# Kernel tuning notes

Hardware: AMD Instinct MI355X
Metric: run time of the kernel (lower is better)

Reference implementation:

```python
import jax, jax.numpy as jnp
import numpy as np

D_MODEL, D_HIDDEN, N_EXPERTS, TOP_K = 1024, 2048, 8, 2


def setup_inputs() -> dict:
    key = jax.random.key(0)
    ks = jax.random.split(key, 8)
    s_in = 1.0 / np.sqrt(D_MODEL)
    s_hid = 1.0 / np.sqrt(D_HIDDEN)
    return {
        "x": jax.random.normal(ks[0], (1, 2048, D_MODEL), dtype=jnp.float32),
        # stacked expert weights, stored (in, out) so y = x @ W + b
        "W1": jax.random.normal(ks[1], (N_EXPERTS, D_MODEL, D_HIDDEN), dtype=jnp.float32) * s_in,
        "b1": jnp.zeros((N_EXPERTS, D_HIDDEN), dtype=jnp.float32),
        "W2": jax.random.normal(ks[2], (N_EXPERTS, D_MODEL, D_HIDDEN), dtype=jnp.float32) * s_in,
        "b2": jnp.zeros((N_EXPERTS, D_HIDDEN), dtype=jnp.float32),
        "Wo": jax.random.normal(ks[3], (N_EXPERTS, D_HIDDEN, D_MODEL), dtype=jnp.float32) * s_hid,
        "bo": jnp.zeros((N_EXPERTS, D_MODEL), dtype=jnp.float32),
        "Wr": jax.random.normal(ks[4], (D_MODEL, N_EXPERTS), dtype=jnp.float32) * s_in,
        "br": jnp.zeros((N_EXPERTS,), dtype=jnp.float32),
    }


def reference(x, W1, b1, W2, b2, Wo, bo, Wr, br):
    B, S, D = x.shape
    T = B * S
    xf = x.reshape(T, D)

    # router
    logits = xf @ Wr + br                      # [T, E]
    probs = jax.nn.softmax(logits, axis=-1)
    topk_probs, topk_idx = jax.lax.top_k(probs, TOP_K)  # [T, K]

    # combine weights: c[t, e] = sum_k topk_probs[t, k] * 1[topk_idx[t, k] == e]
    c = jnp.zeros((T, N_EXPERTS), dtype=xf.dtype)
    c = c.at[jnp.arange(T)[:, None], topk_idx].add(topk_probs)  # [T, E]

    # per-expert SwiGLU FFN applied densely, then masked-combined (same math
    # as the original gather/scatter loop since c[t,e]=0 for unrouted experts)
    h = jnp.einsum('td,edh->eth', xf, W1) + b1[:, None, :]   # [E, T, H]
    g = jnp.einsum('td,edh->eth', xf, W2) + b2[:, None, :]
    y = jnp.einsum('eth,ehd->etd', h * jax.nn.silu(g), Wo) + bo[:, None, :]
    out = jnp.einsum('etd,te->td', y, c).reshape(B, S, D)

    probs_mean = probs.mean(axis=0)
    lb_loss = (probs_mean * probs_mean).sum() * N_EXPERTS
    return out, lb_loss
```

## Files before the change

kernel.cpp:

```cpp
#include <hip/hip_runtime.h>
#include <hip/hip_bf16.h>

#define T_TOK 2048
#define DM 1024
#define DH 2048
#define NE 8
#define MT_MAX 40

using bf16x8 = __attribute__((ext_vector_type(8))) short;
using f32x4  = __attribute__((ext_vector_type(4))) float;

__device__ __forceinline__ unsigned short f2bf(float f) {
  union { float f; unsigned u; } v; v.f = f;
  unsigned r = v.u + 0x7FFFu + ((v.u >> 16) & 1u);
  return (unsigned short)(r >> 16);
}
__device__ __forceinline__ unsigned pk2(float a, float b) {
  return (unsigned)f2bf(a) | ((unsigned)f2bf(b) << 16);
}

#define GLOAD16(gsrc, ldst)                                                        \
  __builtin_amdgcn_global_load_lds(                                                \
      (const __attribute__((address_space(1))) unsigned int*)(gsrc),               \
      (__attribute__((address_space(3))) unsigned int*)(ldst), 16, 0, 0)

__global__ void k_init(int* __restrict__ cnt) {
  if (threadIdx.x < NE) cnt[threadIdx.x] = 0;
}

__global__ __launch_bounds__(256) void k_router(
    const float* __restrict__ x, const float* __restrict__ Wr, const float* __restrict__ br,
    int* __restrict__ cnt, int* __restrict__ idx, float* __restrict__ wgt,
    int* __restrict__ t2r, float* __restrict__ probs, unsigned short* __restrict__ xb)
{
  const int wave = threadIdx.x >> 6, l = threadIdx.x & 63;
  const int t = blockIdx.x * 4 + wave;
  float xv[16];
#pragma unroll
  for (int i = 0; i < 16; ++i) xv[i] = x[t*DM + l + 64*i];
#pragma unroll
  for (int i = 0; i < 16; ++i) xb[t*DM + l + 64*i] = f2bf(xv[i]);

  float acc[8] = {0.f,0.f,0.f,0.f,0.f,0.f,0.f,0.f};
#pragma unroll
  for (int i = 0; i < 16; ++i) {
    const float4* wp = (const float4*)&Wr[(size_t)(l + 64*i)*NE];
    float4 wa = wp[0], wb = wp[1];
    acc[0] += xv[i]*wa.x; acc[1] += xv[i]*wa.y; acc[2] += xv[i]*wa.z; acc[3] += xv[i]*wa.w;
    acc[4] += xv[i]*wb.x; acc[5] += xv[i]*wb.y; acc[6] += xv[i]*wb.z; acc[7] += xv[i]*wb.w;
  }
#pragma unroll
  for (int e = 0; e < 8; ++e) {
#pragma unroll
    for (int off = 32; off; off >>= 1) acc[e] += __shfl_xor(acc[e], off, 64);
    acc[e] += br[e];
  }
  float mx = acc[0];
#pragma unroll
  for (int e = 1; e < 8; ++e) mx = fmaxf(mx, acc[e]);
  float p[8], s = 0.f;
#pragma unroll
  for (int e = 0; e < 8; ++e) { p[e] = expf(acc[e] - mx); s += p[e]; }
  float inv = 1.f / s;
#pragma unroll
  for (int e = 0; e < 8; ++e) p[e] *= inv;

  int e0 = 0; float p0 = p[0];
#pragma unroll
  for (int e = 1; e < 8; ++e) if (p[e] > p0) { p0 = p[e]; e0 = e; }
  int e1 = -1; float p1 = -1.f;
#pragma unroll
  for (int e = 0; e < 8; ++e) { if (e == e0) continue; if (p[e] > p1) { p1 = p[e]; e1 = e; } }

  if (l == 0) {
#pragma unroll
    for (int e = 0; e < 8; ++e) probs[t*NE + e] = p[e];
    int pos0 = atomicAdd(&cnt[e0], 1);
    idx[e0*T_TOK + pos0] = t; wgt[e0*T_TOK + pos0] = p0;
    t2r[t*2 + 0] = e0*T_TOK + pos0;
    int pos1 = atomicAdd(&cnt[e1], 1);
    idx[e1*T_TOK + pos1] = t; wgt[e1*T_TOK + pos1] = p1;
    t2r[t*2 + 1] = e1*T_TOK + pos1;
  }
}

__global__ __launch_bounds__(256) void k_finalize(
    const int* __restrict__ cnt, int* __restrict__ rb,
    const float* __restrict__ probs, float* __restrict__ out,
    int* __restrict__ MTp, int* __restrict__ mtab)
{
  __shared__ float red[8][256];
  const int tid = threadIdx.x;
  float s[8] = {0.f,0.f,0.f,0.f,0.f,0.f,0.f,0.f};
  for (int t = tid; t < T_TOK; t += 256) {
#pragma unroll
    for (int e = 0; e < 8; ++e) s[e] += probs[t*NE + e];
  }
#pragma unroll
  for (int e = 0; e < 8; ++e) red[e][tid] = s[e];
  __syncthreads();
  for (int w = 128; w > 0; w >>= 1) {
    if (tid < w) {
#pragma unroll
      for (int e = 0; e < 8; ++e) red[e][tid] += red[e][tid + w];
    }
    __syncthreads();
  }
  if (tid == 0) {
    float lb = 0.f;
#pragma unroll
    for (int e = 0; e < 8; ++e) {
      float mean = red[e][0] * (1.f / T_TOK);
      lb += mean * mean;
    }
    out[2097152] = lb * NE;
    int r = 0, mc = 0;
#pragma unroll
    for (int e = 0; e < 8; ++e) {
      rb[e] = r; r += cnt[e];
      int nmt = (cnt[e] + 127) / 128;
      for (int j = 0; j < nmt; ++j) mtab[mc++] = (e << 16) | j;
    }
    *MTp = mc;
  }
}

__global__ __launch_bounds__(256) void k_convT(
    const float* __restrict__ in, unsigned short* __restrict__ outT,
    int R, int C, int nnt)
{
  const int e = blockIdx.z;
  const int r0 = blockIdx.y * 64, c0 = blockIdx.x * 64;
  __shared__ float t[64][65];
  const int tid = threadIdx.x;
  const int lr = tid >> 4, lc = (tid & 15) * 4;
#pragma unroll
  for (int i = 0; i < 4; ++i) {
    float4 v = *(const float4*)&in[((size_t)e*R + r0 + lr + i*16)*C + c0 + lc];
    t[lr + i*16][lc+0] = v.x; t[lr + i*16][lc+1] = v.y;
    t[lr + i*16][lc+2] = v.z; t[lr + i*16][lc+3] = v.w;
  }
  __syncthreads();
  const int oc = tid >> 3;
  const int od = (tid & 7) * 8;
  const size_t base2 = ((size_t)e*128 + (size_t)(r0 >> 6)*nnt + (c0 >> 8)) * 16384
                     + (size_t)(c0 & 255) * 64;
#pragma unroll
  for (int i = 0; i < 2; ++i) {
    int c = oc + i*32;
    uint4 v;
    v.x = pk2(t[od+0][c], t[od+1][c]);
    v.y = pk2(t[od+2][c], t[od+3][c]);
    v.z = pk2(t[od+4][c], t[od+5][c]);
    v.w = pk2(t[od+6][c], t[od+7][c]);
    *(uint4*)&outT[base2 + (size_t)c*64 + od] = v;
  }
}

#define TM1 128
#define TN1 64
#define BKK 64

__global__ __launch_bounds__(256) void k_ffn1b(
    const unsigned short* __restrict__ xb,
    const unsigned short* __restrict__ W1T, const float* __restrict__ b1,
    const unsigned short* __restrict__ W2T, const float* __restrict__ b2,
    const int* __restrict__ cnt, const int* __restrict__ rbp,
    const int* __restrict__ idx, unsigned short* __restrict__ act,
    const int* __restrict__ MTp, const int* __restrict__ mtab)
{
  const int mtg = blockIdx.y;
  if (mtg >= *MTp) return;
  const int code = mtab[mtg];
  const int e = code >> 16, mt = code & 0xffff;
  const int Me = cnt[e];
  const int m0 = mt * TM1;
  const int nt = blockIdx.x;
  const int n0 = nt * TN1;

  __shared__ __align__(16) unsigned short As[TM1*BKK];
  __shared__ __align__(16) unsigned short Bh[TN1*BKK];
  __shared__ __align__(16) unsigned short Bg[TN1*BKK];
  __shared__ int toks[TM1];

  const int tid = threadIdx.x;
  if (tid < TM1) toks[tid] = idx[e*T_TOK + min(m0 + tid, Me - 1)];
  __syncthreads();

  const int lane = tid & 63;
  const int wave = tid >> 6;
  const int wm = wave >> 1, wn = wave & 1;
  const int row16 = lane & 15, kg = lane >> 4;
  const int sl = lane & 7;
  const int lr = lane >> 3;

  const unsigned short* asrc[4];
#pragma unroll
  for (int i = 0; i < 4; ++i) {
    int r = (wave*4 + i)*8 + lr;
    asrc[i] = &xb[(size_t)toks[r]*DM + ((sl ^ (r & 7)) * 8)];
  }
  const unsigned short *bsrc1[2], *bsrc2[2];
  const int nt256 = n0 >> 8, nsub = n0 & 255;
#pragma unroll
  for (int j = 0; j < 2; ++j) {
    int r = (wave*2 + j)*8 + lr;
    size_t gb = ((size_t)e*128 + nt256)*16384 + (size_t)(nsub + r)*64 + ((sl ^ (r & 7)) * 8);
    bsrc1[j] = &W1T[gb]; bsrc2[j] = &W2T[gb];
  }

  f32x4 ah[4][2], ag[4][2];
#pragma unroll
  for (int i = 0; i < 4; ++i)
#pragma unroll
    for (int j = 0; j < 2; ++j) { ah[i][j] = 0.f; ag[i][j] = 0.f; }

  for (int k0 = 0; k0 < DM; k0 += BKK) {
    const size_t bko = (size_t)k0 * 2048;
#pragma unroll
    for (int i = 0; i < 4; ++i)
      GLOAD16(asrc[i] + k0, &As[(wave*4 + i)*512]);
#pragma unroll
    for (int j = 0; j < 2; ++j) {
      GLOAD16(bsrc1[j] + bko, &Bh[(wave*2 + j)*512]);
      GLOAD16(bsrc2[j] + bko, &Bg[(wave*2 + j)*512]);
    }
    __syncthreads();
#pragma unroll
    for (int ks = 0; ks < 2; ++ks) {
      const int kslot = ks*4 + kg;
      bf16x8 a[4], vbh[2], vbg[2];
#pragma unroll
      for (int mi = 0; mi < 4; ++mi) {
        int m = wm*64 + mi*16 + row16;
        a[mi] = *(const bf16x8*)&As[m*BKK + ((kslot ^ (m & 7)) * 8)];
      }
#pragma unroll
      for (int ni = 0; ni < 2; ++ni) {
        int n = wn*32 + ni*16 + row16;
        int off = n*BKK + ((kslot ^ (n & 7)) * 8);
        vbh[ni] = *(const bf16x8*)&Bh[off];
        vbg[ni] = *(const bf16x8*)&Bg[off];
      }
#pragma unroll
      for (int mi = 0; mi < 4; ++mi)
#pragma unroll
        for (int ni = 0; ni < 2; ++ni) {
          ah[mi][ni] = __builtin_amdgcn_mfma_f32_16x16x32_bf16(a[mi], vbh[ni], ah[mi][ni], 0, 0, 0);
          ag[mi][ni] = __builtin_amdgcn_mfma_f32_16x16x32_bf16(a[mi], vbg[ni], ag[mi][ni], 0, 0, 0);
        }
    }
    __syncthreads();
  }

  const int rb = rbp[e];
#pragma unroll
  for (int mi = 0; mi < 4; ++mi) {
#pragma unroll
    for (int i = 0; i < 4; ++i) {
      int rloc = wm*64 + mi*16 + (lane >> 4)*4 + i;
      int m = m0 + rloc;
      if (m < Me) {
#pragma unroll
        for (int ni = 0; ni < 2; ++ni) {
          int col = n0 + wn*32 + ni*16 + row16;
          float h = ah[mi][ni][i] + b1[e*DH + col];
          float g = ag[mi][ni][i] + b2[e*DH + col];
          float sg = g / (1.f + __expf(-g));
          act[(size_t)(rb + m)*DH + col] = f2bf(h * sg);
        }
      }
    }
  }
}

__global__ __launch_bounds__(256) void k_ffn2b(
    const unsigned short* __restrict__ act,
    const unsigned short* __restrict__ WoT, const float* __restrict__ bo,
    const int* __restrict__ cnt, const int* __restrict__ rbp,
    float* __restrict__ ys,
    const int* __restrict__ MTp, const int* __restrict__ mtab)
{
  const int mtg = blockIdx.y;
  if (mtg >= *MTp) return;
  const int code = mtab[mtg];
  const int e = code >> 16, mt = code & 0xffff;
  const int Me = cnt[e];
  const int m0 = mt * TM1;
  const int nt = blockIdx.x;
  const int n0 = nt * TN1;
  const int rb = rbp[e];

  __shared__ __align__(16) unsigned short As[TM1*BKK];
  __shared__ __align__(16) unsigned short Bs[TN1*BKK];

  const int tid = threadIdx.x;
  const int lane = tid & 63;
  const int wave = tid >> 6;
  const int wm = wave >> 1, wn = wave & 1;
  const int row16 = lane & 15, kg = lane >> 4;
  const int sl = lane & 7;
  const int lr = lane >> 3;

  const unsigned short* asrc[4];
#pragma unroll
  for (int i = 0; i < 4; ++i) {
    int r = (wave*4 + i)*8 + lr;
    int grow = rb + min(m0 + r, Me - 1);
    asrc[i] = &act[(size_t)grow*DH + ((sl ^ (r & 7)) * 8)];
  }
  const unsigned short* bsrc[2];
  const int nt256 = n0 >> 8, nsub = n0 & 255;
#pragma unroll
  for (int j = 0; j < 2; ++j) {
    int r = (wave*2 + j)*8 + lr;
    size_t gb = ((size_t)e*128 + nt256)*16384 + (size_t)(nsub + r)*64 + ((sl ^ (r & 7)) * 8);
    bsrc[j] = &WoT[gb];
  }

  f32x4 acc[4][2];
#pragma unroll
  for (int i = 0; i < 4; ++i)
#pragma unroll
    for (int j = 0; j < 2; ++j) acc[i][j] = 0.f;

  for (int k0 = 0; k0 < DH; k0 += BKK) {
    const size_t bko = (size_t)k0 * 1024;
#pragma unroll
    for (int i = 0; i < 4; ++i)
      GLOAD16(asrc[i] + k0, &As[(wave*4 + i)*512]);
#pragma unroll
    for (int j = 0; j < 2; ++j)
      GLOAD16(bsrc[j] + bko, &Bs[(wave*2 + j)*512]);
    __syncthreads();
#pragma unroll
    for (int ks = 0; ks < 2; ++ks) {
      const int kslot = ks*4 + kg;
      bf16x8 a[4], b[2];
#pragma unroll
      for (int mi = 0; mi < 4; ++mi) {
        int m = wm*64 + mi*16 + row16;
        a[mi] = *(const bf16x8*)&As[m*BKK + ((kslot ^ (m & 7)) * 8)];
      }
#pragma unroll
      for (int ni = 0; ni < 2; ++ni) {
        int n = wn*32 + ni*16 + row16;
        b[ni] = *(const bf16x8*)&Bs[n*BKK + ((kslot ^ (n & 7)) * 8)];
      }
#pragma unroll
      for (int mi = 0; mi < 4; ++mi)
#pragma unroll
        for (int ni = 0; ni < 2; ++ni)
          acc[mi][ni] = __builtin_amdgcn_mfma_f32_16x16x32_bf16(a[mi], b[ni], acc[mi][ni], 0, 0, 0);
    }
    __syncthreads();
  }

#pragma unroll
  for (int mi = 0; mi < 4; ++mi) {
#pragma unroll
    for (int i = 0; i < 4; ++i) {
      int rloc = wm*64 + mi*16 + (lane >> 4)*4 + i;
      int m = m0 + rloc;
      if (m < Me) {
#pragma unroll
        for (int ni = 0; ni < 2; ++ni) {
          int col = n0 + wn*32 + ni*16 + row16;
          ys[(size_t)(rb + m)*DM + col] = acc[mi][ni][i] + bo[e*DM + col];
        }
      }
    }
  }
}

__global__ __launch_bounds__(256) void k_combine(
    const float* __restrict__ ys, const int* __restrict__ t2r,
    const int* __restrict__ rbp, const float* __restrict__ wgt,
    float* __restrict__ out)
{
  const int t = blockIdx.x, tid = threadIdx.x;
  const int c0 = t2r[t*2 + 0], c1 = t2r[t*2 + 1];
  const float w0 = wgt[c0], w1 = wgt[c1];
  const int r0 = rbp[c0 >> 11] + (c0 & 2047);
  const int r1 = rbp[c1 >> 11] + (c1 & 2047);
  const float4* p0 = (const float4*)&ys[(size_t)r0*DM];
  const float4* p1 = (const float4*)&ys[(size_t)r1*DM];
  float4* po = (float4*)&out[(size_t)t*DM];
  float4 a = p0[tid], b = p1[tid];
  float4 r;
  r.x = w0*a.x + w1*b.x; r.y = w0*a.y + w1*b.y;
  r.z = w0*a.z + w1*b.z; r.w = w0*a.w + w1*b.w;
  po[tid] = r;
}

extern "C" void kernel_launch(void* const* d_in, const int* in_sizes, int n_in,
                              void* d_out, int out_size, void* d_ws, size_t ws_size,
                              hipStream_t stream)
{
  const float* x  = (const float*)d_in[0];
  const float* W1 = (const float*)d_in[1];
  const float* b1 = (const float*)d_in[2];
  const float* W2 = (const float*)d_in[3];
  const float* b2 = (const float*)d_in[4];
  const float* Wo = (const float*)d_in[5];
  const float* bo = (const float*)d_in[6];
  const float* Wr = (const float*)d_in[7];
  const float* br = (const float*)d_in[8];
  float* out = (float*)d_out;

  char* ws = (char*)d_ws;
  int*   cnt   = (int*)(ws + 0);
  int*   rb    = (int*)(ws + 64);
  int*   MTp   = (int*)(ws + 128);
  int*   mtab  = (int*)(ws + 192);
  int*   t2r   = (int*)(ws + 4096);
  int*   idx   = (int*)(ws + 32*1024);
  float* wgt   = (float*)(ws + 96*1024);
  float* probs = (float*)(ws + 160*1024);
  unsigned short* xb  = (unsigned short*)(ws + 256*1024);
  unsigned short* act = (unsigned short*)(ws + 5ull*1024*1024);
  float* ysb = (float*)(ws + 21ull*1024*1024);
  unsigned short* W1T = (unsigned short*)(ws + 40ull*1024*1024);
  unsigned short* W2T = (unsigned short*)(ws + 72ull*1024*1024);
  unsigned short* WoT = (unsigned short*)(ws + 104ull*1024*1024);

  k_init<<<1, 64, 0, stream>>>(cnt);
  k_router<<<T_TOK/4, 256, 0, stream>>>(x, Wr, br, cnt, idx, wgt, t2r, probs, xb);
  k_finalize<<<1, 256, 0, stream>>>(cnt, rb, probs, out, MTp, mtab);
  k_convT<<<dim3(DH/64, DM/64, NE), 256, 0, stream>>>(W1, W1T, DM, DH, 8);
  k_convT<<<dim3(DH/64, DM/64, NE), 256, 0, stream>>>(W2, W2T, DM, DH, 8);
  k_convT<<<dim3(DM/64, DH/64, NE), 256, 0, stream>>>(Wo, WoT, DH, DM, 4);
  k_ffn1b<<<dim3(DH/TN1, MT_MAX), 256, 0, stream>>>(xb, W1T, b1, W2T, b2, cnt, rb, idx, act, MTp, mtab);
  k_ffn2b<<<dim3(DM/TN1, MT_MAX), 256, 0, stream>>>(act, WoT, bo, cnt, rb, ysb, MTp, mtab);
  k_combine<<<T_TOK, 256, 0, stream>>>(ysb, t2r, rb, wgt, out);
}
```

Baseline: 218.5 us.

## Double M-tile to 256 rows with 512-thread blocks and merge weight conversions

```diff
diff --git a/kernel.cpp b/kernel.cpp
--- a/kernel.cpp
+++ b/kernel.cpp
@@ -5,7 +5,7 @@
 #define DM 1024
 #define DH 2048
 #define NE 8
-#define MT_MAX 40
+#define MT_MAX 24
 
 using bf16x8 = __attribute__((ext_vector_type(8))) short;
 using f32x4  = __attribute__((ext_vector_type(4))) float;
@@ -118,19 +118,27 @@
 #pragma unroll
     for (int e = 0; e < 8; ++e) {
       rb[e] = r; r += cnt[e];
-      int nmt = (cnt[e] + 127) / 128;
+      int nmt = (cnt[e] + 255) / 256;
       for (int j = 0; j < nmt; ++j) mtab[mc++] = (e << 16) | j;
     }
     *MTp = mc;
   }
 }
 
-__global__ __launch_bounds__(256) void k_convT(
-    const float* __restrict__ in, unsigned short* __restrict__ outT,
-    int R, int C, int nnt)
-{
-  const int e = blockIdx.z;
-  const int r0 = blockIdx.y * 64, c0 = blockIdx.x * 64;
+__global__ __launch_bounds__(256) void k_convAll(
+    const float* __restrict__ W1, const float* __restrict__ W2, const float* __restrict__ Wo,
+    unsigned short* __restrict__ W1T, unsigned short* __restrict__ W2T,
+    unsigned short* __restrict__ WoT)
+{
+  const int z = blockIdx.z;
+  const float* in; unsigned short* outT; int R, C, nnt, e, r0, c0;
+  if (z < 8)       { in = W1; outT = W1T; R = DM; C = DH; nnt = 8; e = z;
+                     r0 = blockIdx.y * 64; c0 = blockIdx.x * 64; }
+  else if (z < 16) { in = W2; outT = W2T; R = DM; C = DH; nnt = 8; e = z - 8;
+                     r0 = blockIdx.y * 64; c0 = blockIdx.x * 64; }
+  else             { in = Wo; outT = WoT; R = DH; C = DM; nnt = 4; e = z - 16;
+                     r0 = blockIdx.x * 64; c0 = blockIdx.y * 64; }
+
   __shared__ float t[64][65];
   const int tid = threadIdx.x;
   const int lr = tid >> 4, lc = (tid & 15) * 4;
@@ -157,11 +165,11 @@
   }
 }
 
-#define TM1 128
+#define TM2 256
 #define TN1 64
 #define BKK 64
 
-__global__ __launch_bounds__(256) void k_ffn1b(
+__global__ __launch_bounds__(512) void k_ffn1b(
     const unsigned short* __restrict__ xb,
     const unsigned short* __restrict__ W1T, const float* __restrict__ b1,
     const unsigned short* __restrict__ W2T, const float* __restrict__ b2,
@@ -174,17 +182,17 @@
   const int code = mtab[mtg];
   const int e = code >> 16, mt = code & 0xffff;
   const int Me = cnt[e];
-  const int m0 = mt * TM1;
+  const int m0 = mt * TM2;
   const int nt = blockIdx.x;
   const int n0 = nt * TN1;
 
-  __shared__ __align__(16) unsigned short As[TM1*BKK];
+  __shared__ __align__(16) unsigned short As[TM2*BKK];
   __shared__ __align__(16) unsigned short Bh[TN1*BKK];
   __shared__ __align__(16) unsigned short Bg[TN1*BKK];
-  __shared__ int toks[TM1];
+  __shared__ int toks[TM2];
 
   const int tid = threadIdx.x;
-  if (tid < TM1) toks[tid] = idx[e*T_TOK + min(m0 + tid, Me - 1)];
+  if (tid < TM2) toks[tid] = idx[e*T_TOK + min(m0 + tid, Me - 1)];
   __syncthreads();
 
   const int lane = tid & 63;
@@ -200,14 +208,12 @@
     int r = (wave*4 + i)*8 + lr;
     asrc[i] = &xb[(size_t)toks[r]*DM + ((sl ^ (r & 7)) * 8)];
   }
-  const unsigned short *bsrc1[2], *bsrc2[2];
   const int nt256 = n0 >> 8, nsub = n0 & 255;
-#pragma unroll
-  for (int j = 0; j < 2; ++j) {
-    int r = (wave*2 + j)*8 + lr;
-    size_t gb = ((size_t)e*128 + nt256)*16384 + (size_t)(nsub + r)*64 + ((sl ^ (r & 7)) * 8);
-    bsrc1[j] = &W1T[gb]; bsrc2[j] = &W2T[gb];
-  }
+  const int rB = wave*8 + lr;
+  const size_t gbB = ((size_t)e*128 + nt256)*16384 + (size_t)(nsub + rB)*64
+                   + ((sl ^ (rB & 7)) * 8);
+  const unsigned short* bsrc1 = &W1T[gbB];
+  const unsigned short* bsrc2 = &W2T[gbB];
 
   f32x4 ah[4][2], ag[4][2];
 #pragma unroll
@@ -220,11 +226,8 @@
 #pragma unroll
     for (int i = 0; i < 4; ++i)
       GLOAD16(asrc[i] + k0, &As[(wave*4 + i)*512]);
-#pragma unroll
-    for (int j = 0; j < 2; ++j) {
-      GLOAD16(bsrc1[j] + bko, &Bh[(wave*2 + j)*512]);
-      GLOAD16(bsrc2[j] + bko, &Bg[(wave*2 + j)*512]);
-    }
+    GLOAD16(bsrc1 + bko, &Bh[wave*512]);
+    GLOAD16(bsrc2 + bko, &Bg[wave*512]);
     __syncthreads();
 #pragma unroll
     for (int ks = 0; ks < 2; ++ks) {
@@ -274,7 +277,7 @@
   }
 }
 
-__global__ __launch_bounds__(256) void k_ffn2b(
+__global__ __launch_bounds__(512) void k_ffn2b(
     const unsigned short* __restrict__ act,
     const unsigned short* __restrict__ WoT, const float* __restrict__ bo,
     const int* __restrict__ cnt, const int* __restrict__ rbp,
@@ -286,12 +289,12 @@
   const int code = mtab[mtg];
   const int e = code >> 16, mt = code & 0xffff;
   const int Me = cnt[e];
-  const int m0 = mt * TM1;
+  const int m0 = mt * TM2;
   const int nt = blockIdx.x;
   const int n0 = nt * TN1;
   const int rb = rbp[e];
 
-  __shared__ __align__(16) unsigned short As[TM1*BKK];
+  __shared__ __align__(16) unsigned short As[TM2*BKK];
   __shared__ __align__(16) unsigned short Bs[TN1*BKK];
 
   const int tid = threadIdx.x;
@@ -309,14 +312,11 @@
     int grow = rb + min(m0 + r, Me - 1);
     asrc[i] = &act[(size_t)grow*DH + ((sl ^ (r & 7)) * 8)];
   }
-  const unsigned short* bsrc[2];
   const int nt256 = n0 >> 8, nsub = n0 & 255;
-#pragma unroll
-  for (int j = 0; j < 2; ++j) {
-    int r = (wave*2 + j)*8 + lr;
-    size_t gb = ((size_t)e*128 + nt256)*16384 + (size_t)(nsub + r)*64 + ((sl ^ (r & 7)) * 8);
-    bsrc[j] = &WoT[gb];
-  }
+  const int rB = wave*8 + lr;
+  const size_t gbB = ((size_t)e*128 + nt256)*16384 + (size_t)(nsub + rB)*64
+                   + ((sl ^ (rB & 7)) * 8);
+  const unsigned short* bsrc = &WoT[gbB];
 
   f32x4 acc[4][2];
 #pragma unroll
@@ -329,9 +329,7 @@
 #pragma unroll
     for (int i = 0; i < 4; ++i)
       GLOAD16(asrc[i] + k0, &As[(wave*4 + i)*512]);
-#pragma unroll
-    for (int j = 0; j < 2; ++j)
-      GLOAD16(bsrc[j] + bko, &Bs[(wave*2 + j)*512]);
+    GLOAD16(bsrc + bko, &Bs[wave*512]);
     __syncthreads();
 #pragma unroll
     for (int ks = 0; ks < 2; ++ks) {
@@ -427,10 +425,8 @@
   k_init<<<1, 64, 0, stream>>>(cnt);
   k_router<<<T_TOK/4, 256, 0, stream>>>(x, Wr, br, cnt, idx, wgt, t2r, probs, xb);
   k_finalize<<<1, 256, 0, stream>>>(cnt, rb, probs, out, MTp, mtab);
-  k_convT<<<dim3(DH/64, DM/64, NE), 256, 0, stream>>>(W1, W1T, DM, DH, 8);
-  k_convT<<<dim3(DH/64, DM/64, NE), 256, 0, stream>>>(W2, W2T, DM, DH, 8);
-  k_convT<<<dim3(DM/64, DH/64, NE), 256, 0, stream>>>(Wo, WoT, DH, DM, 4);
-  k_ffn1b<<<dim3(DH/TN1, MT_MAX), 256, 0, stream>>>(xb, W1T, b1, W2T, b2, cnt, rb, idx, act, MTp, mtab);
-  k_ffn2b<<<dim3(DM/TN1, MT_MAX), 256, 0, stream>>>(act, WoT, bo, cnt, rb, ysb, MTp, mtab);
+  k_convAll<<<dim3(32, 16, 24), 256, 0, stream>>>(W1, W2, Wo, W1T, W2T, WoT);
+  k_ffn1b<<<dim3(DH/TN1, MT_MAX), 512, 0, stream>>>(xb, W1T, b1, W2T, b2, cnt, rb, idx, act, MTp, mtab);
+  k_ffn2b<<<dim3(DM/TN1, MT_MAX), 512, 0, stream>>>(act, WoT, bo, cnt, rb, ysb, MTp, mtab);
   k_combine<<<T_TOK, 256, 0, stream>>>(ysb, t2r, rb, wgt, out);
 }
```

Measured after the change: 246.0 us. 1.13x slower.

## Fuse expert combine into FFN2 epilogue with weighted atomic adds

Applied to the files above, without the earlier changes.

```diff
diff --git a/kernel.cpp b/kernel.cpp
--- a/kernel.cpp
+++ b/kernel.cpp
@@ -23,10 +23,6 @@
   __builtin_amdgcn_global_load_lds(                                                \
       (const __attribute__((address_space(1))) unsigned int*)(gsrc),               \
       (__attribute__((address_space(3))) unsigned int*)(ldst), 16, 0, 0)
-
-__global__ void k_init(int* __restrict__ cnt) {
-  if (threadIdx.x < NE) cnt[threadIdx.x] = 0;
-}
 
 __global__ __launch_bounds__(256) void k_router(
     const float* __restrict__ x, const float* __restrict__ Wr, const float* __restrict__ br,
@@ -278,7 +274,8 @@
     const unsigned short* __restrict__ act,
     const unsigned short* __restrict__ WoT, const float* __restrict__ bo,
     const int* __restrict__ cnt, const int* __restrict__ rbp,
-    float* __restrict__ ys,
+    const int* __restrict__ idx, const float* __restrict__ wgt,
+    float* __restrict__ out,
     const int* __restrict__ MTp, const int* __restrict__ mtab)
 {
   const int mtg = blockIdx.y;
@@ -293,8 +290,16 @@
 
   __shared__ __align__(16) unsigned short As[TM1*BKK];
   __shared__ __align__(16) unsigned short Bs[TN1*BKK];
+  __shared__ int   toks[TM1];
+  __shared__ float wgts[TM1];
 
   const int tid = threadIdx.x;
+  if (tid < TM1) {
+    int p = min(m0 + tid, Me - 1);
+    toks[tid] = idx[e*T_TOK + p];
+    wgts[tid] = wgt[e*T_TOK + p];
+  }
+
   const int lane = tid & 63;
   const int wave = tid >> 6;
   const int wm = wave >> 1, wn = wave & 1;
@@ -363,34 +368,17 @@
       int rloc = wm*64 + mi*16 + (lane >> 4)*4 + i;
       int m = m0 + rloc;
       if (m < Me) {
+        const int t = toks[rloc];
+        const float w = wgts[rloc];
 #pragma unroll
         for (int ni = 0; ni < 2; ++ni) {
           int col = n0 + wn*32 + ni*16 + row16;
-          ys[(size_t)(rb + m)*DM + col] = acc[mi][ni][i] + bo[e*DM + col];
+          float y = acc[mi][ni][i] + bo[e*DM + col];
+          atomicAdd(&out[(size_t)t*DM + col], w * y);
         }
       }
     }
   }
-}
-
-__global__ __launch_bounds__(256) void k_combine(
-    const float* __restrict__ ys, const int* __restrict__ t2r,
-    const int* __restrict__ rbp, const float* __restrict__ wgt,
-    float* __restrict__ out)
-{
-  const int t = blockIdx.x, tid = threadIdx.x;
-  const int c0 = t2r[t*2 + 0], c1 = t2r[t*2 + 1];
-  const float w0 = wgt[c0], w1 = wgt[c1];
-  const int r0 = rbp[c0 >> 11] + (c0 & 2047);
-  const int r1 = rbp[c1 >> 11] + (c1 & 2047);
-  const float4* p0 = (const float4*)&ys[(size_t)r0*DM];
-  const float4* p1 = (const float4*)&ys[(size_t)r1*DM];
-  float4* po = (float4*)&out[(size_t)t*DM];
-  float4 a = p0[tid], b = p1[tid];
-  float4 r;
-  r.x = w0*a.x + w1*b.x; r.y = w0*a.y + w1*b.y;
-  r.z = w0*a.z + w1*b.z; r.w = w0*a.w + w1*b.w;
-  po[tid] = r;
 }
 
 extern "C" void kernel_launch(void* const* d_in, const int* in_sizes, int n_in,
@@ -419,18 +407,17 @@
   float* probs = (float*)(ws + 160*1024);
   unsigned short* xb  = (unsigned short*)(ws + 256*1024);
   unsigned short* act = (unsigned short*)(ws + 5ull*1024*1024);
-  float* ysb = (float*)(ws + 21ull*1024*1024);
   unsigned short* W1T = (unsigned short*)(ws + 40ull*1024*1024);
   unsigned short* W2T = (unsigned short*)(ws + 72ull*1024*1024);
   unsigned short* WoT = (unsigned short*)(ws + 104ull*1024*1024);
 
-  k_init<<<1, 64, 0, stream>>>(cnt);
+  hipMemsetAsync(out, 0, (size_t)out_size * sizeof(float), stream);
+  hipMemsetAsync(cnt, 0, NE * sizeof(int), stream);
   k_router<<<T_TOK/4, 256, 0, stream>>>(x, Wr, br, cnt, idx, wgt, t2r, probs, xb);
   k_finalize<<<1, 256, 0, stream>>>(cnt, rb, probs, out, MTp, mtab);
   k_convT<<<dim3(DH/64, DM/64, NE), 256, 0, stream>>>(W1, W1T, DM, DH, 8);
   k_convT<<<dim3(DH/64, DM/64, NE), 256, 0, stream>>>(W2, W2T, DM, DH, 8);
   k_convT<<<dim3(DM/64, DH/64, NE), 256, 0, stream>>>(Wo, WoT, DH, DM, 4);
   k_ffn1b<<<dim3(DH/TN1, MT_MAX), 256, 0, stream>>>(xb, W1T, b1, W2T, b2, cnt, rb, idx, act, MTp, mtab);
-  k_ffn2b<<<dim3(DM/TN1, MT_MAX), 256, 0, stream>>>(act, WoT, bo, cnt, rb, ysb, MTp, mtab);
-  k_combine<<<T_TOK, 256, 0, stream>>>(ysb, t2r, rb, wgt, out);
-}
+  k_ffn2b<<<dim3(DM/TN1, MT_MAX), 256, 0, stream>>>(act, WoT, bo, cnt, rb, idx, wgt, out, MTp, mtab);
+}
```

After: 223.5 us. +2.3%, slower.
